# Performance work log

Measured on AMD Instinct MI355X. Metric: run time of the kernel, lower is better.

The kernel has to match this reference:

```python
import jax, jax.numpy as jnp
import numpy as np

HEADS = 8


def setup_inputs() -> dict:
    key = jax.random.key(0)
    ks = jax.random.split(key, 6)
    dim = 256
    s = 0.02
    return {
        "x": jax.random.normal(ks[0], (8, dim, 32, 32), jnp.float32),
        "w_qkv": jax.random.normal(ks[1], (3 * dim, dim), jnp.float32) * s,
        "w_out": jax.random.normal(ks[2], (dim, dim), jnp.float32) * s,
        "b_out": jnp.zeros((dim,), jnp.float32),
        "w_g1": jax.random.normal(ks[3], (dim // 4, dim), jnp.float32) * s,
        "b_g1": jnp.zeros((dim // 4,), jnp.float32),
        "w_g2": jax.random.normal(ks[4], (1, dim // 4), jnp.float32) * s,
        "b_g2": jnp.zeros((1,), jnp.float32),
    }


def _conv1x1(t, w, bias=None):
    # 1x1 conv == channel matmul
    y = jnp.einsum('bchw,oc->bohw', t, w)
    if bias is not None:
        y = y + bias[None, :, None, None]
    return y


def _forward(x, w_qkv, w_out, b_out, w_g1, b_g1, w_g2, b_g2):
    b, c, h, w = x.shape
    heads = HEADS
    d = c // heads
    n = h * w
    m = min(h, w)
    scale = d ** (-0.5)

    qkv = _conv1x1(x, w_qkv)  # [b, 3c, h, w]

    def to_heads(t):  # 'b (h d) x y -> b h (x y) d'
        return t.reshape(b, heads, d, n).transpose(0, 1, 3, 2)

    q, k, v = (to_heads(t) for t in jnp.split(qkv, 3, axis=1))

    attn = jax.nn.softmax(jnp.einsum('bhid,bhjd->bhij', q, k) * scale, axis=-1)

    # diagonal branch (anti-diagonal scores are computed in the original but
    # never used in the output -> omitted as dead code)
    q2d = q.reshape(b, heads, h, w, d)
    k2d = k.reshape(b, heads, h, w, d)
    q_dm = jnp.diagonal(q2d, axis1=2, axis2=3)  # [b, heads, d, m]
    k_dm = jnp.diagonal(k2d, axis1=2, axis2=3)
    diag_main = jnp.einsum('bhnd,bhmd->bhnm', q_dm, k_dm) * scale  # [b, heads, d, d]
    diag_vec = jnp.diagonal(diag_main.mean(axis=1), axis1=-2, axis2=-1)  # [b, d]
    diag_vec = jnp.pad(diag_vec, ((0, 0), (0, n - m)))  # [b, n] (d == m)

    DIAG_WEIGHT = 0.3
    enhanced = attn + DIAG_WEIGHT * diag_vec[:, None, :, None]

    out = jnp.einsum('bhij,bhjd->bhid', enhanced, v)  # [b, heads, n, d]
    out = out.reshape(b, heads, h, w, d).transpose(0, 1, 4, 2, 3).reshape(b, c, h, w)

    # left/right asymmetry gate
    mid = w // 2
    left = x[:, :, :, :mid]
    right = x[:, :, :, mid:]
    asym = jnp.abs(left - right[:, :, :, ::-1])  # [b, c, h, w/2]
    # adaptive_avg_pool2d (h, w/2) -> (h, w) with even w == width repeat by 2
    pooled = jnp.repeat(asym, 2, axis=3)
    g = _conv1x1(pooled, w_g1, b_g1)
    g = jax.nn.gelu(g, approximate=False)
    g = jax.nn.sigmoid(_conv1x1(g, w_g2, b_g2))  # [b, 1, h, w]

    out = out * (1.0 + g)
    return _conv1x1(out, w_out, b_out)


def reference(x, w_qkv, w_out, b_out, w_g1, b_g1, w_g2, b_g2):
    return _forward(x, w_qkv, w_out, b_out, w_g1, b_g1, w_g2, b_g2)
```

## Files before the change

kernel.cpp:

```cpp
#include <hip/hip_runtime.h>
#include <hip/hip_bf16.h>
#include <math.h>

#define B 8
#define C 256
#define HEADS 8
#define D 32
#define NPIX 1024
#define OC 768
#define SCALE 0.17677669529663687f
#define LOG2E 1.4426950408889634f

typedef unsigned int uint;
typedef unsigned short u16;
typedef __attribute__((ext_vector_type(8))) short bf16x8;
typedef __attribute__((ext_vector_type(4))) short bf16x4;
typedef __attribute__((ext_vector_type(4))) float f32x4;

static __device__ inline u16 f2bf(float f) {
  uint u = __float_as_uint(f);
  return (u16)((u + 0x7fffu + ((u >> 16) & 1u)) >> 16);
}
static __device__ inline float bfval(u16 v) { return __uint_as_float((uint)v << 16); }
static __device__ inline float bf_lo(uint u) { return __uint_as_float(u << 16); }
static __device__ inline float bf_hi(uint u) { return __uint_as_float(u & 0xffff0000u); }

static __device__ inline uint pk2(float lo, float hi) {
  union { __hip_bfloat162 h; uint u; } cv;
  cv.h = __float22bfloat162_rn(float2{lo, hi});
  return cv.u;
}

__global__ __launch_bounds__(256) void k_prep_gate(
    const float* __restrict__ x, const float* __restrict__ wqkv,
    const float* __restrict__ wout,
    const float* __restrict__ wg1, const float* __restrict__ bg1,
    const float* __restrict__ wg2, const float* __restrict__ bg2,
    u16* __restrict__ WQ, u16* __restrict__ WO, u16* __restrict__ XT,
    float* __restrict__ gate) {
  const int bid = blockIdx.x, t = threadIdx.x;
  __shared__ float smem[16 * 257 + 16 * 65];
  if (bid < 256) {
    const float* src;
    u16* dst;
    int base;
    if (bid < 192) { src = wqkv; dst = WQ; base = bid * 1024; }
    else           { src = wout; dst = WO; base = (bid - 192) * 1024; }
    float4 v = *(const float4*)(src + base + t * 4);
    uint2 pk = make_uint2((uint)f2bf(v.x) | ((uint)f2bf(v.y) << 16),
                          (uint)f2bf(v.z) | ((uint)f2bf(v.w) << 16));
    *(uint2*)(dst + base + t * 4) = pk;
    return;
  }
  if (bid < 768) {
    u16 (*tile)[65] = (u16(*)[65])smem;
    const int id = bid - 256;
    const int pt = id & 15, ct = (id >> 4) & 3, b = id >> 6;
    {
      const int px = t & 63, cq = t >> 6;
      const float* xb = x + ((size_t)(b * C + ct * 64)) * NPIX + pt * 64;
#pragma unroll
      for (int m = 0; m < 16; ++m) {
        const int c = cq * 16 + m;
        tile[c][px] = f2bf(xb[(size_t)c * NPIX + px]);
      }
    }
    __syncthreads();
    {
      const int cc = t & 63, pq = t >> 6;
      const int c = ct * 64 + cc;
      const int kc = c >> 5, quad = (c >> 3) & 3, mm = c & 7;
      u16* dst = XT + ((size_t)((b * 64 + pt * 4 + pq) * 8 + kc) * 512 +
                       quad * 128 + mm);
#pragma unroll
      for (int m = 0; m < 16; ++m)
        dst[m * 8] = tile[cc][pq * 16 + m];
    }
    return;
  }
  const int id = bid - 768;
  const int h = id & 31, b = id >> 5;
  float* pl = smem;
  float* gl = smem + 16 * 257;
  {
    const int c = t;
    const float* row = x + ((size_t)(b * C + c) * NPIX + h * 32);
    float v[32];
#pragma unroll
    for (int m = 0; m < 32; ++m) v[m] = row[m];
#pragma unroll
    for (int k = 0; k < 16; ++k) pl[k * 257 + c] = fabsf(v[k] - v[31 - k]);
  }
  __syncthreads();

  const int o16 = t >> 4, k = t & 15;
#pragma unroll 1
  for (int p = 0; p < 4; ++p) {
    const int o = p * 16 + o16;
    const float* wr = wg1 + o * C;
    float a0 = 0.f, a1 = 0.f, a2 = 0.f, a3 = 0.f;
#pragma unroll 4
    for (int c = 0; c < C; c += 4) {
      a0 += wr[c]     * pl[k * 257 + c];
      a1 += wr[c + 1] * pl[k * 257 + c + 1];
      a2 += wr[c + 2] * pl[k * 257 + c + 2];
      a3 += wr[c + 3] * pl[k * 257 + c + 3];
    }
    float a = bg1[o] + ((a0 + a1) + (a2 + a3));
    gl[k * 65 + o] = 0.5f * a * (1.f + erff(a * 0.70710678118654752f));
  }
  __syncthreads();

  if (t < 16) {
    float s = bg2[0];
    for (int o = 0; o < 64; ++o)
      s += wg2[o] * gl[t * 65 + o];
    gate[(b * 32 + h) * 16 + t] = 1.f / (1.f + expf(-s));
  }
}

__global__ __launch_bounds__(256) void k_qkv_mfma(
    const u16* __restrict__ XTF, const u16* __restrict__ WQ,
    u16* __restrict__ Q, u16* __restrict__ Kk, u16* __restrict__ VT) {
  const int ob = blockIdx.x, pb = blockIdx.y, b = blockIdx.z;
  const int t = threadIdx.x;
  const int wv = t >> 6, lane = t & 63;
  const int quad = lane >> 4, l15 = lane & 15;
  const int part = ob >> 2;
  const int odl = (ob & 3) * 64 + wv * 16;
  const int hh = odl >> 5, d0 = odl & 31;
  const int bh = b * HEADS + hh;
  const int pix0 = pb * 128;

  __shared__ u16 sb[2][4096];

  const u16* arow = WQ + (size_t)(ob * 64 + wv * 16 + l15) * C;
  bf16x8 af[8];
#pragma unroll
  for (int kc = 0; kc < 8; ++kc)
    af[kc] = *(const bf16x8*)(arow + kc * 32 + quad * 8);

  const u16* xb = XTF + (size_t)(b * 64 + pb * 8) * 8 * 512;
  const int snt = t >> 5, si = (t & 31) * 16;

  f32x4 acc[8];
#pragma unroll
  for (int nt = 0; nt < 8; ++nt) acc[nt] = (f32x4){0.f, 0.f, 0.f, 0.f};

  {
    const u16* p = xb + (size_t)(snt * 8 + 0) * 512 + si;
    uint4 r0 = *(const uint4*)(p);
    uint4 r1 = *(const uint4*)(p + 8);
    u16* d = &sb[0][snt * 512 + si];
    *(uint4*)(d) = r0;
    *(uint4*)(d + 8) = r1;
  }
  __syncthreads();

  int cur = 0;
  for (int kc = 0; kc < 8; ++kc) {
    uint4 r0, r1;
    if (kc < 7) {
      const u16* p = xb + (size_t)(snt * 8 + kc + 1) * 512 + si;
      r0 = *(const uint4*)(p);
      r1 = *(const uint4*)(p + 8);
    }
    const u16* s = &sb[cur][0];
#pragma unroll
    for (int nt = 0; nt < 8; ++nt) {
      bf16x8 bfr = *(const bf16x8*)(s + nt * 512 + lane * 8);
      acc[nt] = __builtin_amdgcn_mfma_f32_16x16x32_bf16(af[kc], bfr, acc[nt], 0, 0, 0);
    }
    if (kc < 7) {
      u16* d = &sb[cur ^ 1][snt * 512 + si];
      *(uint4*)(d) = r0;
      *(uint4*)(d + 8) = r1;
    }
    __syncthreads();
    cur ^= 1;
  }

  if (part == 0) {
    const float qs = SCALE * LOG2E;
    u16* dst = Q + (size_t)bh * NPIX * D;
#pragma unroll
    for (int nt = 0; nt < 8; ++nt) {
      const int pix = pix0 + nt * 16 + l15;
      uint2 pk = make_uint2(
          (uint)f2bf(acc[nt][0] * qs) | ((uint)f2bf(acc[nt][1] * qs) << 16),
          (uint)f2bf(acc[nt][2] * qs) | ((uint)f2bf(acc[nt][3] * qs) << 16));
      *(uint2*)(dst + (size_t)pix * D + d0 + 4 * quad) = pk;
    }
  } else if (part == 1) {
    u16* kfb = Kk + (size_t)bh * NPIX * D;
    const int lane_k8 = (((d0 >> 3) + (quad >> 1)) * 16 + l15) * 8 + (quad & 1) * 4;
#pragma unroll
    for (int nt = 0; nt < 8; ++nt) {
      uint2 pk = make_uint2(
          (uint)f2bf(acc[nt][0]) | ((uint)f2bf(acc[nt][1]) << 16),
          (uint)f2bf(acc[nt][2]) | ((uint)f2bf(acc[nt][3]) << 16));
      *(uint2*)(kfb + (size_t)(pb * 8 + nt) * 512 + lane_k8) = pk;
    }
  } else {
    u16* vb = VT + (size_t)bh * NPIX * D;
#pragma unroll
    for (int nt = 0; nt < 8; ++nt) {
      const int pix = pix0 + nt * 16 + l15;
      const int jb16 = pix >> 4, qa = (pix >> 2) & 3, m = pix & 3;
#pragma unroll
      for (int r = 0; r < 4; ++r) {
        const int d = d0 + 4 * quad + r;
        const int nta = d >> 4, l15a = d & 15;
        vb[((size_t)(jb16 * 2 + nta) * 64 + qa * 16 + l15a) * 4 + m] =
            f2bf(acc[nt][r]);
      }
    }
  }
}

__global__ __launch_bounds__(256) void k_red(
    const u16* __restrict__ Q, const u16* __restrict__ KF,
    const u16* __restrict__ VT, float* __restrict__ diagv,
    float* __restrict__ colsum) {
  const int bid = blockIdx.x, tid = threadIdx.x;
  __shared__ float red[256];
  if (bid < 8) {
    const int b = bid;
    const int hh = tid >> 5, dd = tid & 31;
    const u16* qb = Q + (size_t)(b * HEADS + hh) * NPIX * D;
    const u16* kb = KF + (size_t)(b * HEADS + hh) * NPIX * D;
    float s = 0.f;
#pragma unroll 4
    for (int t = 0; t < 32; ++t) {
      const int j = t * 33;
      float qv = bfval(qb[(size_t)j * D + dd]);
      float kv = bfval(kb[(size_t)(j >> 4) * 512 +
                          ((dd >> 3) * 16 + (j & 15)) * 8 + (dd & 7)]);
      s += qv * kv;
    }
    red[tid] = s;
    __syncthreads();
    if (tid < 32) {
      float v = 0.f;
#pragma unroll
      for (int h8 = 0; h8 < 8; ++h8) v += red[h8 * 32 + tid];
      diagv[b * 32 + tid] = v * (0.125f / LOG2E);
    }
  } else {
    const int bh = bid - 8;
    const int d = tid >> 3, sl = tid & 7;
    const int nta = d >> 4, l15a = d & 15;
    const u16* vb = VT + (size_t)bh * NPIX * D;
    float s = 0.f;
    for (int jb = 0; jb < 8; ++jb) {
      const int jb16 = sl * 8 + jb;
#pragma unroll
      for (int qa = 0; qa < 4; ++qa) {
        const uint2 u = *(const uint2*)(
            vb + ((size_t)(jb16 * 2 + nta) * 64 + qa * 16 + l15a) * 4);
        s += bf_lo(u.x) + bf_hi(u.x) + bf_lo(u.y) + bf_hi(u.y);
      }
    }
    red[tid] = s;
    __syncthreads();
    if (tid < 32) {
      float v = 0.f;
#pragma unroll
      for (int g = 0; g < 8; ++g) v += red[tid * 8 + g];
      colsum[bh * D + tid] = v;
    }
  }
}

__global__ __launch_bounds__(512, 4) void k_attn(
    const u16* __restrict__ Q, const u16* __restrict__ KF,
    const u16* __restrict__ VF, const float* __restrict__ diagv,
    const float* __restrict__ colsum, u16* __restrict__ AOT) {
  const int qc = blockIdx.x;
  const int bh = blockIdx.y;
  const int b = bh >> 3, hh = bh & 7;
  const int wv = threadIdx.x >> 6, lane = threadIdx.x & 63;
  const int quad = lane >> 4, l15 = lane & 15;
  const int i0 = qc * 128 + wv * 16;

  __shared__ u16 sbuf[2][4096];

  const u16* Qb  = Q  + (size_t)bh * NPIX * D;
  const u16* KFb = KF + (size_t)bh * NPIX * D;
  const u16* VFb = VF + (size_t)bh * NPIX * D;

  bf16x8 qfrag = *(const bf16x8*)(Qb + (size_t)(i0 + l15) * D + quad * 8);

  f32x4 oacc[2];
  oacc[0] = (f32x4){0.f, 0.f, 0.f, 0.f};
  oacc[1] = (f32x4){0.f, 0.f, 0.f, 0.f};
  float lacc[4] = {};

  const int soff = (wv >= 4 ? 2048 : 0) + (wv & 3) * 512 + lane * 8;
  const u16* gsrc = (wv < 4 ? KFb : VFb) + (wv & 3) * 512 + lane * 8;
  u16* ldst0 = &sbuf[0][soff];
  u16* ldst1 = &sbuf[1][soff];

  *(uint4*)(ldst0) = *(const uint4*)(gsrc);
  __syncthreads();

  int cur = 0;
  for (int it = 0; it < 16; ++it) {
    uint4 pre;
    if (it < 15)
      pre = *(const uint4*)(gsrc + (size_t)(it + 1) * 2048);
    const u16* sK = cur ? &sbuf[1][0] : &sbuf[0][0];
    const u16* sV = sK + 2048;

    f32x4 st[4];
#pragma unroll
    for (int jt = 0; jt < 4; ++jt) {
      bf16x8 kfrag = *(const bf16x8*)(sK + jt * 512 + lane * 8);
      st[jt] = __builtin_amdgcn_mfma_f32_16x16x32_bf16(
          kfrag, qfrag, (f32x4){0.f, 0.f, 0.f, 0.f}, 0, 0, 0);
    }

#pragma unroll
    for (int jt = 0; jt < 4; ++jt)
#pragma unroll
      for (int r = 0; r < 4; ++r) {
        float pv = exp2f(fminf(st[jt][r], 80.f));
        lacc[r] += pv;
        st[jt][r] = pv;
      }

    __builtin_amdgcn_s_setprio(1);
#pragma unroll
    for (int jt = 0; jt < 4; ++jt) {
      union { uint u[2]; bf16x4 v; } pa;
      pa.u[0] = pk2(st[jt][0], st[jt][1]);
      pa.u[1] = pk2(st[jt][2], st[jt][3]);
#pragma unroll
      for (int nt = 0; nt < 2; ++nt) {
        bf16x4 vfr = *(const bf16x4*)(sV + (jt * 2 + nt) * 256 + lane * 4);
        oacc[nt] = __builtin_amdgcn_mfma_f32_16x16x16bf16_1k(
            pa.v, vfr, oacc[nt], 0, 0, 0);
      }
    }
    __builtin_amdgcn_s_setprio(0);

    if (it < 15)
      *(uint4*)(cur ? ldst0 : ldst1) = pre;
    __syncthreads();
    cur ^= 1;
  }

  float lt = (lacc[0] + lacc[1]) + (lacc[2] + lacc[3]);
  lt += __shfl_xor(lt, 16, 64);
  lt += __shfl_xor(lt, 32, 64);
  const float linv = 1.f / lt;
  float rinv[4];
#pragma unroll
  for (int r = 0; r < 4; ++r) rinv[r] = __shfl(linv, quad * 4 + r, 64);

  const bool do_diag = (i0 < 32);
  const int p16 = i0 >> 4;
  u16* aobase = AOT + ((size_t)(b * 64 + p16) * 8 + hh) * 512 + (l15 & 7);
  const int hi8 = l15 >> 3;
#pragma unroll
  for (int nt = 0; nt < 2; ++nt) {
    const int qa = nt * 2 + hi8;
    float cs = do_diag ? colsum[bh * D + (nt * 16 + l15)] : 0.f;
#pragma unroll
    for (int r = 0; r < 4; ++r) {
      const int irow = i0 + quad * 4 + r;
      float o = oacc[nt][r] * rinv[r];
      if (do_diag) o += 0.3f * diagv[b * 32 + irow] * cs;
      aobase[(qa * 16 + quad * 4 + r) * 8] = f2bf(o);
    }
  }
}

__global__ __launch_bounds__(256) void k_out_mfma(
    const u16* __restrict__ AOF, const u16* __restrict__ WO,
    const float* __restrict__ bout, const float* __restrict__ gate,
    float* __restrict__ out) {
  const int ob = blockIdx.x, pb = blockIdx.y, b = blockIdx.z;
  const int wv = threadIdx.x >> 6, lane = threadIdx.x & 63;
  const int quad = lane >> 4, l15 = lane & 15;
  const int o0 = ob * 64 + wv * 16;
  const int pix0 = pb * 128;

  const u16* arow = WO + (size_t)(o0 + l15) * C;
  bf16x8 af[8];
#pragma unroll
  for (int kc = 0; kc < 8; ++kc)
    af[kc] = *(const bf16x8*)(arow + kc * 32 + quad * 8);

  const u16* ab = AOF + (size_t)(b * 64 + pb * 8) * 8 * 512 + lane * 8;
  f32x4 acc[8];
#pragma unroll
  for (int nt = 0; nt < 8; ++nt) acc[nt] = (f32x4){0.f, 0.f, 0.f, 0.f};

  for (int kc = 0; kc < 8; ++kc) {
#pragma unroll
    for (int nt = 0; nt < 8; ++nt) {
      bf16x8 bfr = *(const bf16x8*)(ab + (size_t)(nt * 8 + kc) * 512);
      acc[nt] = __builtin_amdgcn_mfma_f32_16x16x32_bf16(af[kc], bfr, acc[nt], 0, 0, 0);
    }
  }

#pragma unroll
  for (int nt = 0; nt < 8; ++nt) {
    const int pix = pix0 + nt * 16 + l15;
    const float gf = 1.f + gate[(b * 32 + (pix >> 5)) * 16 + ((pix & 31) >> 1)];
#pragma unroll
    for (int r = 0; r < 4; ++r) {
      const int o = o0 + 4 * quad + r;
      out[((size_t)b * C + o) * NPIX + pix] = acc[nt][r] * gf + bout[o];
    }
  }
}

extern "C" void kernel_launch(void* const* d_in, const int* in_sizes, int n_in,
                              void* d_out, int out_size, void* d_ws, size_t ws_size,
                              hipStream_t stream) {
  const float* x    = (const float*)d_in[0];
  const float* wqkv = (const float*)d_in[1];
  const float* wout = (const float*)d_in[2];
  const float* bout = (const float*)d_in[3];
  const float* wg1  = (const float*)d_in[4];
  const float* bg1  = (const float*)d_in[5];
  const float* wg2  = (const float*)d_in[6];
  const float* bg2  = (const float*)d_in[7];
  float* out = (float*)d_out;

  const size_t SZ = (size_t)B * HEADS * NPIX * D;
  u16* XT = (u16*)d_ws;
  u16* WQ = XT + SZ;
  u16* WO = WQ + (size_t)OC * C;
  u16* Q  = WO + (size_t)C * C;
  u16* Kq = Q + SZ;
  u16* VT = Kq + SZ;
  float* DIAG = (float*)(VT + SZ);
  float* COL  = DIAG + 256;
  float* GATE = COL + 2048;
  u16* AOT = XT;

  hipLaunchKernelGGL(k_prep_gate, dim3(1024), dim3(256), 0, stream,
                     x, wqkv, wout, wg1, bg1, wg2, bg2, WQ, WO, XT, GATE);
  hipLaunchKernelGGL(k_qkv_mfma, dim3(12, 8, B), dim3(256), 0, stream,
                     XT, WQ, Q, Kq, VT);
  hipLaunchKernelGGL(k_red, dim3(72), dim3(256), 0, stream,
                     Q, Kq, VT, DIAG, COL);
  hipLaunchKernelGGL(k_attn, dim3(8, 64), dim3(512), 0, stream,
                     Q, Kq, VT, DIAG, COL, AOT);
  hipLaunchKernelGGL(k_out_mfma, dim3(4, 8, B), dim3(256), 0, stream,
                     AOT, WO, bout, GATE, out);
}
```

Baseline: 144.8 us.

## Double K/V tile size in attention and stage AO tiles through LDS in output GEMM

The attention kernel now loads 128-key K/V tiles per iteration instead of 64, halving the loop trips and barriers at the cost of twice the shared memory per block. The output projection kernel now stages the shared AO activation tile in double-buffered LDS, loaded cooperatively once per block. Previously each of the four waves read that tile from global memory on its own. The larger LDS footprint in attention may reduce how many blocks fit on a CU.

```diff
diff --git a/kernel.cpp b/kernel.cpp
--- a/kernel.cpp
+++ b/kernel.cpp
@@ -283,7 +283,7 @@
   const int quad = lane >> 4, l15 = lane & 15;
   const int i0 = qc * 128 + wv * 16;
 
-  __shared__ u16 sbuf[2][4096];
+  __shared__ u16 sbuf[2][8192];
 
   const u16* Qb  = Q  + (size_t)bh * NPIX * D;
   const u16* KFb = KF + (size_t)bh * NPIX * D;
@@ -296,56 +296,70 @@
   oacc[1] = (f32x4){0.f, 0.f, 0.f, 0.f};
   float lacc[4] = {};
 
-  const int soff = (wv >= 4 ? 2048 : 0) + (wv & 3) * 512 + lane * 8;
-  const u16* gsrc = (wv < 4 ? KFb : VFb) + (wv & 3) * 512 + lane * 8;
-  u16* ldst0 = &sbuf[0][soff];
-  u16* ldst1 = &sbuf[1][soff];
-
-  *(uint4*)(ldst0) = *(const uint4*)(gsrc);
+  const int soff = (wv >= 4 ? 4096 : 0) + (wv & 3) * 1024 + lane * 16;
+  const u16* gsrc = (wv < 4 ? KFb : VFb) + (wv & 3) * 1024 + lane * 16;
+
+  {
+    uint4 a0 = *(const uint4*)(gsrc);
+    uint4 a1 = *(const uint4*)(gsrc + 8);
+    *(uint4*)(&sbuf[0][soff]) = a0;
+    *(uint4*)(&sbuf[0][soff + 8]) = a1;
+  }
   __syncthreads();
 
   int cur = 0;
-  for (int it = 0; it < 16; ++it) {
-    uint4 pre;
-    if (it < 15)
-      pre = *(const uint4*)(gsrc + (size_t)(it + 1) * 2048);
-    const u16* sK = cur ? &sbuf[1][0] : &sbuf[0][0];
-    const u16* sV = sK + 2048;
-
-    f32x4 st[4];
-#pragma unroll
-    for (int jt = 0; jt < 4; ++jt) {
-      bf16x8 kfrag = *(const bf16x8*)(sK + jt * 512 + lane * 8);
-      st[jt] = __builtin_amdgcn_mfma_f32_16x16x32_bf16(
-          kfrag, qfrag, (f32x4){0.f, 0.f, 0.f, 0.f}, 0, 0, 0);
-    }
-
-#pragma unroll
-    for (int jt = 0; jt < 4; ++jt)
-#pragma unroll
-      for (int r = 0; r < 4; ++r) {
-        float pv = exp2f(fminf(st[jt][r], 80.f));
-        lacc[r] += pv;
-        st[jt][r] = pv;
+  for (int it = 0; it < 8; ++it) {
+    uint4 p0, p1;
+    if (it < 7) {
+      const u16* g = gsrc + (size_t)(it + 1) * 4096;
+      p0 = *(const uint4*)(g);
+      p1 = *(const uint4*)(g + 8);
+    }
+    const u16* base = cur ? &sbuf[1][0] : &sbuf[0][0];
+
+#pragma unroll
+    for (int h2 = 0; h2 < 2; ++h2) {
+      const u16* sK = base + h2 * 2048;
+      const u16* sV = base + 4096 + h2 * 2048;
+
+      f32x4 st[4];
+#pragma unroll
+      for (int jt = 0; jt < 4; ++jt) {
+        bf16x8 kfrag = *(const bf16x8*)(sK + jt * 512 + lane * 8);
+        st[jt] = __builtin_amdgcn_mfma_f32_16x16x32_bf16(
+            kfrag, qfrag, (f32x4){0.f, 0.f, 0.f, 0.f}, 0, 0, 0);
       }
 
-    __builtin_amdgcn_s_setprio(1);
-#pragma unroll
-    for (int jt = 0; jt < 4; ++jt) {
-      union { uint u[2]; bf16x4 v; } pa;
-      pa.u[0] = pk2(st[jt][0], st[jt][1]);
-      pa.u[1] = pk2(st[jt][2], st[jt][3]);
-#pragma unroll
-      for (int nt = 0; nt < 2; ++nt) {
-        bf16x4 vfr = *(const bf16x4*)(sV + (jt * 2 + nt) * 256 + lane * 4);
-        oacc[nt] = __builtin_amdgcn_mfma_f32_16x16x16bf16_1k(
-            pa.v, vfr, oacc[nt], 0, 0, 0);
+#pragma unroll
+      for (int jt = 0; jt < 4; ++jt)
+#pragma unroll
+        for (int r = 0; r < 4; ++r) {
+          float pv = exp2f(fminf(st[jt][r], 80.f));
+          lacc[r] += pv;
+          st[jt][r] = pv;
+        }
+
+      __builtin_amdgcn_s_setprio(1);
+#pragma unroll
+      for (int jt = 0; jt < 4; ++jt) {
+        union { uint u[2]; bf16x4 v; } pa;
+        pa.u[0] = pk2(st[jt][0], st[jt][1]);
+        pa.u[1] = pk2(st[jt][2], st[jt][3]);
+#pragma unroll
+        for (int nt = 0; nt < 2; ++nt) {
+          bf16x4 vfr = *(const bf16x4*)(sV + (jt * 2 + nt) * 256 + lane * 4);
+          oacc[nt] = __builtin_amdgcn_mfma_f32_16x16x16bf16_1k(
+              pa.v, vfr, oacc[nt], 0, 0, 0);
+        }
       }
-    }
-    __builtin_amdgcn_s_setprio(0);
-
-    if (it < 15)
-      *(uint4*)(cur ? ldst0 : ldst1) = pre;
+      __builtin_amdgcn_s_setprio(0);
+    }
+
+    if (it < 7) {
+      u16* d = cur ? &sbuf[0][soff] : &sbuf[1][soff];
+      *(uint4*)(d) = p0;
+      *(uint4*)(d + 8) = p1;
+    }
     __syncthreads();
     cur ^= 1;
   }
@@ -381,28 +395,58 @@
     const float* __restrict__ bout, const float* __restrict__ gate,
     float* __restrict__ out) {
   const int ob = blockIdx.x, pb = blockIdx.y, b = blockIdx.z;
-  const int wv = threadIdx.x >> 6, lane = threadIdx.x & 63;
+  const int t = threadIdx.x;
+  const int wv = t >> 6, lane = t & 63;
   const int quad = lane >> 4, l15 = lane & 15;
   const int o0 = ob * 64 + wv * 16;
   const int pix0 = pb * 128;
 
+  __shared__ u16 sb[2][4096];
+
   const u16* arow = WO + (size_t)(o0 + l15) * C;
   bf16x8 af[8];
 #pragma unroll
   for (int kc = 0; kc < 8; ++kc)
     af[kc] = *(const bf16x8*)(arow + kc * 32 + quad * 8);
 
-  const u16* ab = AOF + (size_t)(b * 64 + pb * 8) * 8 * 512 + lane * 8;
+  const u16* ab = AOF + (size_t)(b * 64 + pb * 8) * 8 * 512;
+  const int snt = t >> 5, si = (t & 31) * 16;
+
   f32x4 acc[8];
 #pragma unroll
   for (int nt = 0; nt < 8; ++nt) acc[nt] = (f32x4){0.f, 0.f, 0.f, 0.f};
 
+  {
+    const u16* p = ab + (size_t)(snt * 8 + 0) * 512 + si;
+    uint4 r0 = *(const uint4*)(p);
+    uint4 r1 = *(const uint4*)(p + 8);
+    u16* d = &sb[0][snt * 512 + si];
+    *(uint4*)(d) = r0;
+    *(uint4*)(d + 8) = r1;
+  }
+  __syncthreads();
+
+  int cur = 0;
   for (int kc = 0; kc < 8; ++kc) {
+    uint4 r0, r1;
+    if (kc < 7) {
+      const u16* p = ab + (size_t)(snt * 8 + kc + 1) * 512 + si;
+      r0 = *(const uint4*)(p);
+      r1 = *(const uint4*)(p + 8);
+    }
+    const u16* s = &sb[cur][0];
 #pragma unroll
     for (int nt = 0; nt < 8; ++nt) {
-      bf16x8 bfr = *(const bf16x8*)(ab + (size_t)(nt * 8 + kc) * 512);
+      bf16x8 bfr = *(const bf16x8*)(s + nt * 512 + lane * 8);
       acc[nt] = __builtin_amdgcn_mfma_f32_16x16x32_bf16(af[kc], bfr, acc[nt], 0, 0, 0);
     }
+    if (kc < 7) {
+      u16* d = &sb[cur ^ 1][snt * 512 + si];
+      *(uint4*)(d) = r0;
+      *(uint4*)(d + 8) = r1;
+    }
+    __syncthreads();
+    cur ^= 1;
   }
 
 #pragma unroll
```

Result: no change. 144.8 us (-0.0%).
